# Kernel optimization log

Measured on AMD Instinct MI355X. Metric: run time of the kernel, lower is better.

Reference implementation:

```python
import jax, jax.numpy as jnp
import numpy as np
import itertools, math

# Static config (matches init_kwargs)
DIM = 384
KEY_DIM = 16
NUM_HEADS = 8
ATTN_RATIO = 4
RES = 14
OUT_DIM = 768
RES2 = math.ceil(RES / 2)          # 7
N = RES * RES                      # 196
N2 = RES2 * RES2                   # 49
D = ATTN_RATIO * KEY_DIM           # 64
NH_KD = NUM_HEADS * KEY_DIM        # 128
DH = NUM_HEADS * D                 # 512
SCALE = KEY_DIM ** -0.5
BATCH = 512


def _build_bias_idxs():
    points = list(itertools.product(range(RES), range(RES)))
    points_ = list(itertools.product(range(RES2), range(RES2)))
    ratio = math.ceil(RES / RES2)
    offsets = {}
    idxs = []
    for p1 in points_:
        for p2 in points:
            off = (abs(p1[0] * ratio - p2[0]), abs(p1[1] * ratio - p2[1]))
            if off not in offsets:
                offsets[off] = len(offsets)
            idxs.append(offsets[off])
    return np.array(idxs, dtype=np.int32).reshape(N2, N), len(offsets)


def setup_inputs() -> dict:
    key = jax.random.key(0)
    ks = jax.random.split(key, 16)
    idxs_np, n_off = _build_bias_idxs()
    w = lambda k, shape, s=0.05: (jax.random.normal(k, shape, jnp.float32) * s)
    inp = {
        "x": jax.random.normal(ks[0], (BATCH, DIM, RES, RES), jnp.float32),
        # LGQuery: depthwise 3x3 s2 conv (groups=DIM), then 1x1 conv + BN (folded scale/shift)
        "q_local_w": w(ks[1], (DIM, 1, 3, 3)),
        "q_local_b": w(ks[2], (DIM,)),
        "q_proj_w": w(ks[3], (NH_KD, DIM)),
        "q_proj_b": w(ks[4], (NH_KD,)),
        "q_bn_s": 1.0 + w(ks[5], (NH_KD,)),
        "q_bn_t": w(ks[5], (NH_KD,)),
        # k: 1x1 conv + BN
        "k_w": w(ks[6], (NH_KD, DIM)),
        "k_b": w(ks[7], (NH_KD,)),
        "k_bn_s": 1.0 + w(ks[8], (NH_KD,)),
        "k_bn_t": w(ks[8], (NH_KD,)),
        # v: 1x1 conv + BN
        "v_w": w(ks[9], (DH, DIM)),
        "v_b": w(ks[10], (DH,)),
        "v_bn_s": 1.0 + w(ks[10], (DH,)),
        "v_bn_t": w(ks[10], (DH,)),
        # v_local: depthwise 3x3 s2 (groups=DH) + BN
        "vl_w": w(ks[11], (DH, 1, 3, 3)),
        "vl_b": w(ks[12], (DH,)),
        "vl_bn_s": 1.0 + w(ks[12], (DH,)),
        "vl_bn_t": w(ks[12], (DH,)),
        # proj: GELU -> 1x1 conv -> BN
        "p_w": w(ks[13], (OUT_DIM, DH)),
        "p_b": w(ks[14], (OUT_DIM,)),
        "p_bn_s": 1.0 + w(ks[14], (OUT_DIM,)),
        "p_bn_t": w(ks[14], (OUT_DIM,)),
        # learned relative-position biases + gather indices
        "attn_biases": w(ks[15], (NUM_HEADS, n_off), 0.02),
        "bias_idxs": jnp.asarray(idxs_np),  # [N2, N] int32
    }
    return inp


def _dwconv_s2(x, w, b):
    # depthwise 3x3, stride 2, pad 1, NCHW
    C = x.shape[1]
    y = jax.lax.conv_general_dilated(
        x, w, window_strides=(2, 2), padding=((1, 1), (1, 1)),
        feature_group_count=C, dimension_numbers=("NCHW", "OIHW", "NCHW"))
    return y + b[None, :, None, None]


def _conv1x1_bn(x, w, b, s, t):
    y = jnp.einsum("bchw,oc->bohw", x, w) + b[None, :, None, None]
    return y * s[None, :, None, None] + t[None, :, None, None]


def reference(x, q_local_w, q_local_b, q_proj_w, q_proj_b, q_bn_s, q_bn_t,
              k_w, k_b, k_bn_s, k_bn_t, v_w, v_b, v_bn_s, v_bn_t,
              vl_w, vl_b, vl_bn_s, vl_bn_t, p_w, p_b, p_bn_s, p_bn_t,
              attn_biases, bias_idxs):
    B = x.shape[0]
    # LGQuery: depthwise conv + avgpool(k=1,s=2)==stride subsample, then 1x1+BN
    ql = _dwconv_s2(x, q_local_w, q_local_b) + x[:, :, ::2, ::2]
    q = _conv1x1_bn(ql, q_proj_w, q_proj_b, q_bn_s, q_bn_t)        # [B,128,7,7]
    q = q.reshape(B, NUM_HEADS, KEY_DIM, N2).transpose(0, 1, 3, 2)  # bhqc

    k = _conv1x1_bn(x, k_w, k_b, k_bn_s, k_bn_t).reshape(B, NUM_HEADS, KEY_DIM, N)  # bhck

    v4 = _conv1x1_bn(x, v_w, v_b, v_bn_s, v_bn_t)                   # [B,512,14,14]
    v_local = _dwconv_s2(v4, vl_w, vl_b)
    v_local = v_local * vl_bn_s[None, :, None, None] + vl_bn_t[None, :, None, None]
    v = v4.reshape(B, NUM_HEADS, D, N).transpose(0, 1, 3, 2)        # bhkd

    bias = attn_biases[:, bias_idxs]                                # [H,N2,N]
    attn = jax.nn.softmax(jnp.einsum("bhqc,bhck->bhqk", q, k) * SCALE + bias[None], axis=-1)
    out = jnp.einsum("bhqk,bhkd->bhqd", attn, v)                    # [B,H,N2,D]
    out = out.transpose(0, 1, 3, 2).reshape(B, DH, RES2, RES2) + v_local
    out = jax.nn.gelu(out, approximate=False)                       # torch nn.GELU default (erf)
    out = _conv1x1_bn(out, p_w, p_b, p_bn_s, p_bn_t)                # [B,768,7,7]
    return out
```

## Files before the change

### kernel.cpp

```cpp
#include <hip/hip_runtime.h>
#include <math.h>

#define DIM 384
#define NUM_HEADS 8
#define RES 14
#define RES2 7
#define NPOS 196
#define N2 49
#define DHEAD 64
#define NH_KD 128
#define DH 512
#define OUT_DIM 768
#define BATCH 512
#define SCALE_Q 0.25f

typedef unsigned short u16;
typedef short s16x8 __attribute__((ext_vector_type(8)));
typedef short s16x4 __attribute__((ext_vector_type(4)));
typedef float f32x4 __attribute__((ext_vector_type(4)));
typedef unsigned int u32x2 __attribute__((ext_vector_type(2)));

__device__ __forceinline__ float bf2f(u16 u) {
  union { unsigned int i; float f; } v; v.i = ((unsigned int)u) << 16; return v.f;
}
__device__ __forceinline__ u16 f2bf(float f) {
  union { unsigned int i; float f; } v; v.f = f;
  unsigned int r = v.i + 0x7fffu + ((v.i >> 16) & 1u);
  return (u16)(r >> 16);
}

#define GLD16(gp, lp) __builtin_amdgcn_global_load_lds( \
    (const __attribute__((address_space(1))) void*)(gp), \
    (__attribute__((address_space(3))) void*)(lp), 16, 0, 0)

__global__ __launch_bounds__(256) void k_prep(const float* __restrict__ kw, const float* __restrict__ vw,
                                              const float* __restrict__ qw, const float* __restrict__ pw,
                                              const float* __restrict__ ab, const int* __restrict__ idxs, int noff,
                                              u16* __restrict__ kwb, u16* __restrict__ vwb,
                                              u16* __restrict__ qwb, u16* __restrict__ pwb,
                                              float* __restrict__ bxp) {
  int i = blockIdx.x * 256 + threadIdx.x;
  const int e1 = NH_KD * DIM;
  const int e2 = e1 + DH * DIM;
  const int e3 = e2 + NH_KD * DIM;
  const int e4 = e3 + OUT_DIM * DH;
  const int e5 = e4 + NUM_HEADS * N2 * 256;
  if (i < e1) kwb[i] = f2bf(kw[i]);
  else if (i < e2) vwb[i - e1] = f2bf(vw[i - e1]);
  else if (i < e3) qwb[i - e2] = f2bf(qw[i - e2]);
  else if (i < e4) pwb[i - e3] = f2bf(pw[i - e3]);
  else if (i < e5) {
    int j = i - e4;
    int f = j & 15, c = (j >> 4) & 15;
    int m = (j >> 8) % N2, h = j / (N2 * 256);
    int n = f * 16 + c;
    bxp[j] = (n < NPOS) ? ab[h * noff + idxs[m * NPOS + n]] : 0.f;
  }
}

__global__ __launch_bounds__(256) void k_transpose_dwq(const float* __restrict__ x, u16* __restrict__ xt,
                                                       const float* __restrict__ qlw, const float* __restrict__ qlb,
                                                       u16* __restrict__ qlt) {
  int b = blockIdx.y, c0 = blockIdx.x * 64;
  __shared__ __align__(8) u16 tileT[196 * 70];
  __shared__ float wlds2[576];
  __shared__ float blds[64];
  int tid = threadIdx.x;
  const float* xb = x + (size_t)b * DIM * NPOS;

  for (int idx = tid; idx < 64 * 49; idx += 256) {
    int ch = idx / 49, p4 = idx - ch * 49;
    f32x4 v = *(const f32x4*)(xb + (size_t)(c0 + ch) * NPOS + p4 * 4);
#pragma unroll
    for (int j = 0; j < 4; j++)
      tileT[(p4 * 4 + j) * 70 + ch] = f2bf(v[j]);
  }
  for (int i = tid; i < 576; i += 256) {
    int c = i / 9, t = i % 9;
    wlds2[t * 64 + c] = qlw[(size_t)(c0 + c) * 9 + t];
  }
  if (tid < 64) blds[tid] = qlb[c0 + tid];
  __syncthreads();

  u16* xtb = xt + (size_t)b * NPOS * DIM + c0;
  for (int idx = tid; idx < NPOS * 8; idx += 256) {
    int n = idx >> 3, g = (idx & 7) << 3;
    s16x8 val;
    ((uint*)&val)[0] = *(const uint*)&tileT[n * 70 + g];
    ((uint*)&val)[1] = *(const uint*)&tileT[n * 70 + g + 2];
    ((uint*)&val)[2] = *(const uint*)&tileT[n * 70 + g + 4];
    ((uint*)&val)[3] = *(const uint*)&tileT[n * 70 + g + 6];
    *(s16x8*)(xtb + (size_t)n * DIM + g) = val;
  }
  u16* qb = qlt + (size_t)b * N2 * DIM + c0;
  for (int idx = tid; idx < N2 * 32; idx += 256) {
    int cp = idx & 31, n2 = idx >> 5;
    int c = cp << 1;
    int r = n2 / RES2, s = n2 % RES2;
    uint rv = *(const uint*)&tileT[((2 * r) * RES + 2 * s) * 70 + c];
    float a0 = blds[c]     + bf2f((u16)(rv & 0xffff));
    float a1 = blds[c + 1] + bf2f((u16)(rv >> 16));
#pragma unroll
    for (int dy = 0; dy < 3; dy++) {
      int ry = 2 * r - 1 + dy;
      if (ry < 0 || ry >= RES) continue;
#pragma unroll
      for (int dx = 0; dx < 3; dx++) {
        int sx = 2 * s - 1 + dx;
        if (sx < 0 || sx >= RES) continue;
        uint tv = *(const uint*)&tileT[(ry * RES + sx) * 70 + c];
        int t = dy * 3 + dx;
        a0 += wlds2[t * 64 + c]     * bf2f((u16)(tv & 0xffff));
        a1 += wlds2[t * 64 + c + 1] * bf2f((u16)(tv >> 16));
      }
    }
    uint outp = (uint)f2bf(a0) | ((uint)f2bf(a1) << 16);
    *(uint*)(qb + (size_t)n2 * DIM + c) = outp;
  }
}

template <int SPLN, bool F32OUT>
__global__ __launch_bounds__(256) void k_gemm_flat(
    const u16* __restrict__ A, const u16* __restrict__ B, void* __restrict__ C,
    const float* __restrict__ cb, const float* __restrict__ bns, const float* __restrict__ bnt,
    int K, int NMT, int ldc, long bstride) {
  __shared__ __align__(16) u16 a_lds[2 * 128 * 32];
  __shared__ __align__(16) u16 b_lds[2 * 128 * 32];
  int nwg = gridDim.x, bx = blockIdx.x;
  int wg = ((nwg & 7) == 0) ? ((bx & 7) * (nwg >> 3) + (bx >> 3)) : bx;
  int mt = wg % NMT, nt = wg / NMT;
  int m0 = mt * 128, n0 = nt * 128;
  int tid = threadIdx.x, w = tid >> 6, l = tid & 63;

  int srow = l >> 2;
  int scol = ((l & 3) ^ ((l >> 3) & 3)) * 8;
  const u16* asrc[2]; const u16* bsrc[2];
#pragma unroll
  for (int c = 0; c < 2; c++) {
    int chunk = w * 2 + c;
    asrc[c] = A + (size_t)(m0 + chunk * 16 + srow) * K + scol;
    bsrc[c] = B + (size_t)(n0 + chunk * 16 + srow) * K + scol;
  }
  char* adst = (char*)a_lds + (w * 2) * 1024 + l * 16;
  char* bdst = (char*)b_lds + (w * 2) * 1024 + l * 16;

  f32x4 acc[4][4];
#pragma unroll
  for (int i = 0; i < 4; i++)
#pragma unroll
    for (int j = 0; j < 4; j++) acc[i][j] = (f32x4){0.f, 0.f, 0.f, 0.f};

  int wm = w >> 1, wn = w & 1;
  int rg8 = ((l >> 4) ^ ((l >> 1) & 3)) * 8;
  int arow = wm * 64 + (l & 15);
  int brow = wn * 64 + (l & 15);

  for (int kk = 0; kk < K; kk += 64) {
#pragma unroll
    for (int c = 0; c < 2; c++) {
      GLD16(asrc[c] + kk,      adst + c * 1024);
      GLD16(asrc[c] + kk + 32, adst + 8192 + c * 1024);
      GLD16(bsrc[c] + kk,      bdst + c * 1024);
      GLD16(bsrc[c] + kk + 32, bdst + 8192 + c * 1024);
    }
    __syncthreads();
#pragma unroll
    for (int hf = 0; hf < 2; hf++) {
      const u16* ah = a_lds + hf * (128 * 32);
      const u16* bh = b_lds + hf * (128 * 32);
      s16x8 af[4], bf[4];
#pragma unroll
      for (int i = 0; i < 4; i++) {
        af[i] = *(const s16x8*)(&ah[(arow + i * 16) * 32 + rg8]);
        bf[i] = *(const s16x8*)(&bh[(brow + i * 16) * 32 + rg8]);
      }
#pragma unroll
      for (int i = 0; i < 4; i++)
#pragma unroll
        for (int j = 0; j < 4; j++)
          acc[i][j] = __builtin_amdgcn_mfma_f32_16x16x32_bf16(af[i], bf[j], acc[i][j], 0, 0, 0);
    }
    __syncthreads();
  }

  int ncol = l & 15, mq = (l >> 4) * 4;
#pragma unroll
  for (int i = 0; i < 4; i++) {
#pragma unroll
    for (int j = 0; j < 4; j++) {
      int n = n0 + wn * 64 + j * 16 + ncol;
#pragma unroll
      for (int r = 0; r < 4; r++) {
        int m = m0 + wm * 64 + i * 16 + mq + r;
        int ch = SPLN ? m : n;
        float val = acc[i][j][r] * bns[ch] + (cb[ch] * bns[ch] + bnt[ch]);
        size_t o;
        if (SPLN) o = (size_t)(n / SPLN) * bstride + (size_t)m * SPLN + (n % SPLN);
        else      o = (size_t)m * ldc + n;
        if (F32OUT) ((float*)C)[o] = val;
        else        ((u16*)C)[o] = f2bf(val);
      }
    }
  }
}

__global__ __launch_bounds__(256) void k_dwconv_v(const u16* __restrict__ v4, const float* __restrict__ w,
    const float* __restrict__ bias, const float* __restrict__ bns, const float* __restrict__ bnt,
    u16* __restrict__ vlt) {
  int b = blockIdx.y, ct = blockIdx.x;
  __shared__ u16 tile[64][196];
  int tid = threadIdx.x, wave = tid >> 6, lane = tid & 63;
  const u16* vbp = v4 + ((size_t)b * DH + ct * 64) * NPOS;
  for (int r = wave; r < 64; r += 4) {
    const u16* row = vbp + (size_t)r * NPOS;
    tile[r][lane]       = row[lane];
    tile[r][lane + 64]  = row[lane + 64];
    tile[r][lane + 128] = row[lane + 128];
    if (lane < 4) tile[r][lane + 192] = row[lane + 192];
  }
  __syncthreads();
  for (int idx = tid; idx < 64 * N2; idx += 256) {
    int cl = idx & 63, n2 = idx >> 6;
    int ch = ct * 64 + cl;
    int r = n2 / RES2, s = n2 % RES2;
    float acc = bias[ch];
#pragma unroll
    for (int dy = 0; dy < 3; dy++) {
      int ry = 2 * r - 1 + dy;
      if (ry < 0 || ry >= RES) continue;
#pragma unroll
      for (int dx = 0; dx < 3; dx++) {
        int sx = 2 * s - 1 + dx;
        if (sx < 0 || sx >= RES) continue;
        acc += w[ch * 9 + dy * 3 + dx] * bf2f(tile[cl][ry * RES + sx]);
      }
    }
    vlt[((size_t)b * N2 + n2) * DH + ch] = f2bf(acc * bns[ch] + bnt[ch]);
  }
}

__global__ __launch_bounds__(256, 4) void k_attn_mfma(const u16* __restrict__ qT, const u16* __restrict__ kT,
    const u16* __restrict__ v4, const float* __restrict__ bxp, const u16* __restrict__ vlT,
    u16* __restrict__ gT) {
  int h = blockIdx.x, b = blockIdx.y;
  __shared__ __align__(16) u16 p_lds[64 * 232];
  float* o_lds = (float*)p_lds;
  int tid = threadIdx.x, w = tid >> 6, l = tid & 63;
  int part = l >> 4, row16 = l & 15;
  int mbase = w * 16 + part * 4;
  int ncol = l & 15;

  for (int idx = tid; idx < 64 * 8; idx += 256)
    ((uint*)&p_lds[(idx >> 3) * 232])[104 + (idx & 7)] = 0;

  s16x8 af = (s16x8){0, 0, 0, 0, 0, 0, 0, 0};
  if (part < 2)
    af = *(const s16x8*)(qT + ((size_t)b * N2 + (w * 16 + row16)) * NH_KD + h * 16 + part * 8);

  const u16* kbase = kT + (size_t)b * NPOS * NH_KD + h * 16 + part * 8;
  f32x4 s[13];
#pragma unroll
  for (int f = 0; f < 13; f++) {
    s16x8 bf = (s16x8){0, 0, 0, 0, 0, 0, 0, 0};
    if (part < 2)
      bf = *(const s16x8*)(kbase + (size_t)(f * 16 + row16) * NH_KD);
    s[f] = __builtin_amdgcn_mfma_f32_16x16x32_bf16(af, bf, (f32x4){0.f, 0.f, 0.f, 0.f}, 0, 0, 0);
  }

  const u16* vbase = v4 + ((size_t)b * DH + h * DHEAD) * NPOS;
  int vd = l & 15, vq8 = part * 8;
  auto VLOAD = [&](int f, int kk) {
    const u16* p = vbase + (size_t)(f * 16 + vd) * NPOS + kk + vq8;
    s16x8 r;
    ((u32x2*)&r)[0] = *(const u32x2*)(p);
    ((u32x2*)&r)[1] = *(const u32x2*)(p + 4);
    return r;
  };
  s16x8 vb0[4];
#pragma unroll
  for (int f = 0; f < 4; f++) vb0[f] = VLOAD(f, 0);

#pragma unroll
  for (int q = 0; q < 4; q++) {
    f32x4 bqr[4];
#pragma unroll
    for (int r = 0; r < 4; r++) {
      int mm = mbase + r; if (mm > N2 - 1) mm = N2 - 1;
      bqr[r] = *(const f32x4*)(bxp + (((size_t)h * N2 + mm) * 16 + ncol) * 16 + q * 4);
    }
#pragma unroll
    for (int ff = 0; ff < 4; ff++) {
      int f = q * 4 + ff;
      if (f < 13) {
        int n = f * 16 + ncol;
#pragma unroll
        for (int r = 0; r < 4; r++) {
          int m = mbase + r;
          s[f][r] = (m < N2 && n < NPOS) ? s[f][r] * SCALE_Q + bqr[r][ff] : -1e30f;
        }
      }
    }
  }
#pragma unroll
  for (int r = 0; r < 4; r++) {
    float mx = s[0][r];
#pragma unroll
    for (int f = 1; f < 13; f++) mx = fmaxf(mx, s[f][r]);
    mx = fmaxf(mx, __shfl_xor(mx, 1)); mx = fmaxf(mx, __shfl_xor(mx, 2));
    mx = fmaxf(mx, __shfl_xor(mx, 4)); mx = fmaxf(mx, __shfl_xor(mx, 8));
    float sum = 0.f;
#pragma unroll
    for (int f = 0; f < 13; f++) { s[f][r] = __expf(s[f][r] - mx); sum += s[f][r]; }
    sum += __shfl_xor(sum, 1); sum += __shfl_xor(sum, 2);
    sum += __shfl_xor(sum, 4); sum += __shfl_xor(sum, 8);
    float inv = 1.f / sum;
#pragma unroll
    for (int f = 0; f < 13; f++) s[f][r] *= inv;
  }
#pragma unroll
  for (int f = 0; f < 13; f++) {
    int n = f * 16 + ncol;
#pragma unroll
    for (int r = 0; r < 4; r++)
      p_lds[(mbase + r) * 232 + n] = f2bf(s[f][r]);
  }
  __syncthreads();

  f32x4 o[4];
#pragma unroll
  for (int f = 0; f < 4; f++) o[f] = (f32x4){0.f, 0.f, 0.f, 0.f};
#pragma unroll
  for (int t = 0; t < 7; t++) {
    int kk = t * 32;
    s16x8 vn[4];
    if (t < 6) {
#pragma unroll
      for (int f = 0; f < 4; f++) vn[f] = VLOAD(f, kk + 32);
    }
    s16x8 pa = *(const s16x8*)(&p_lds[(w * 16 + row16) * 232 + kk + part * 8]);
#pragma unroll
    for (int f = 0; f < 4; f++)
      o[f] = __builtin_amdgcn_mfma_f32_16x16x32_bf16(pa, vb0[f], o[f], 0, 0, 0);
    if (t < 6) {
#pragma unroll
      for (int f = 0; f < 4; f++) vb0[f] = vn[f];
    }
  }
  __syncthreads();

#pragma unroll
  for (int f = 0; f < 4; f++)
#pragma unroll
    for (int r = 0; r < 4; r++) {
      int m = mbase + r;
      if (m < N2) o_lds[m * 68 + f * 16 + ncol] = o[f][r];
    }
  __syncthreads();

  for (int idx = tid; idx < N2 * 16; idx += 256) {
    int row = idx >> 4, c4 = (idx & 15) << 2;
    f32x4 ov = *(const f32x4*)(&o_lds[row * 68 + c4]);
    size_t go = ((size_t)b * N2 + row) * DH + h * DHEAD + c4;
    s16x4 vv = *(const s16x4*)(vlT + go);
    s16x4 outv;
#pragma unroll
    for (int e = 0; e < 4; e++) {
      float xv = ov[e] + bf2f((u16)vv[e]);
      float g = 0.5f * xv * (1.f + erff(xv * 0.70710678118f));
      outv[e] = (short)f2bf(g);
    }
    *(s16x4*)(gT + go) = outv;
  }
}

extern "C" void kernel_launch(void* const* d_in, const int* in_sizes, int n_in,
                              void* d_out, int out_size, void* d_ws, size_t ws_size,
                              hipStream_t stream) {
  const float* x   = (const float*)d_in[0];
  const float* qlw = (const float*)d_in[1];
  const float* qlb = (const float*)d_in[2];
  const float* qpw = (const float*)d_in[3];
  const float* qpb = (const float*)d_in[4];
  const float* qbs = (const float*)d_in[5];
  const float* qbt = (const float*)d_in[6];
  const float* kw  = (const float*)d_in[7];
  const float* kb  = (const float*)d_in[8];
  const float* kbs = (const float*)d_in[9];
  const float* kbt = (const float*)d_in[10];
  const float* vw  = (const float*)d_in[11];
  const float* vb  = (const float*)d_in[12];
  const float* vbs = (const float*)d_in[13];
  const float* vbt = (const float*)d_in[14];
  const float* vlw = (const float*)d_in[15];
  const float* vlb = (const float*)d_in[16];
  const float* vls = (const float*)d_in[17];
  const float* vlt_in = (const float*)d_in[18];
  const float* pw  = (const float*)d_in[19];
  const float* pb  = (const float*)d_in[20];
  const float* pbs = (const float*)d_in[21];
  const float* pbt = (const float*)d_in[22];
  const float* ab  = (const float*)d_in[23];
  const int*   bidx = (const int*)d_in[24];
  int noff = in_sizes[23] / NUM_HEADS;

  char* ws = (char*)d_ws;
  size_t off = 0;
  auto alloc = [&](size_t bytes) { char* p = ws + off; off += (bytes + 255) & ~(size_t)255; return p; };
  u16* xbT = (u16*)alloc((size_t)BATCH * NPOS * DIM * 2);
  u16* kTm = (u16*)alloc((size_t)BATCH * NPOS * NH_KD * 2);
  u16* qlT = (u16*)alloc((size_t)BATCH * N2 * DIM * 2);
  u16* qTm = (u16*)alloc((size_t)BATCH * N2 * NH_KD * 2);
  u16* v4m = (u16*)alloc((size_t)BATCH * DH * NPOS * 2);
  u16* vlTm = (u16*)alloc((size_t)BATCH * N2 * DH * 2);
  float* bxp = (float*)alloc((size_t)NUM_HEADS * N2 * 16 * 16 * 4);
  u16* kwb = (u16*)alloc((size_t)NH_KD * DIM * 2);
  u16* vwb = (u16*)alloc((size_t)DH * DIM * 2);
  u16* qwb = (u16*)alloc((size_t)NH_KD * DIM * 2);
  u16* pwb = (u16*)alloc((size_t)OUT_DIM * DH * 2);
  u16* gTm = xbT;

  k_prep<<<(788480 + 255) / 256, 256, 0, stream>>>(kw, vw, qpw, pw, ab, bidx, noff,
                                                   kwb, vwb, qwb, pwb, bxp);

  k_transpose_dwq<<<dim3(6, BATCH), 256, 0, stream>>>(x, xbT, qlw, qlb, qlT);

  k_gemm_flat<0, false><<<784, 256, 0, stream>>>(
      xbT, kwb, kTm, kb, kbs, kbt, DIM, 784, NH_KD, 0);
  k_gemm_flat<NPOS, false><<<3136, 256, 0, stream>>>(
      vwb, xbT, v4m, vb, vbs, vbt, DIM, 4, 0, (long)DH * NPOS);
  k_gemm_flat<0, false><<<196, 256, 0, stream>>>(
      qlT, qwb, qTm, qpb, qbs, qbt, DIM, 196, NH_KD, 0);

  k_dwconv_v<<<dim3(8, BATCH), 256, 0, stream>>>(v4m, vlw, vlb, vls, vlt_in, vlTm);
  k_attn_mfma<<<dim3(NUM_HEADS, BATCH), 256, 0, stream>>>(qTm, kTm, v4m, bxp, vlTm, gTm);

  k_gemm_flat<N2, true><<<1176, 256, 0, stream>>>(
      pwb, gTm, d_out, pb, pbs, pbt, DH, 6, 0, (long)OUT_DIM * N2);
}
```

Baseline: 379.5 us.

## Load small weight operand directly from global, vectorize dwconv tile load, fast GELU

Adds an ADIRECT mode to the flat GEMM in which the A operand (the small weight matrix) is read straight from global/L2 into registers, bypassing LDS staging. This cuts LDS traffic and the A-side load instructions for the V projection and the output projection. The depthwise conv tile load now uses 8-byte vector loads instead of scalar u16 loads. The exact erf GELU is replaced with an Abramowitz-Stegun polynomial approximation using a hardware reciprocal and fast exp, which trades a small accuracy loss for fewer instructions.

```diff
diff --git a/kernel.cpp b/kernel.cpp
--- a/kernel.cpp
+++ b/kernel.cpp
@@ -27,6 +27,17 @@
   union { unsigned int i; float f; } v; v.f = f;
   unsigned int r = v.i + 0x7fffu + ((v.i >> 16) & 1u);
   return (u16)(r >> 16);
+}
+
+__device__ __forceinline__ float gelu_f(float x) {
+  float z = x * 0.70710678118f;
+  float az = fabsf(z);
+  float t = __builtin_amdgcn_rcpf(1.f + 0.3275911f * az);
+  float p = ((((1.061405429f * t - 1.453152027f) * t + 1.421413741f) * t
+              - 0.284496736f) * t + 0.254829592f) * t;
+  float erfv = 1.f - p * __expf(-az * az);
+  erfv = copysignf(erfv, z);
+  return 0.5f * x * (1.f + erfv);
 }
 
 #define GLD16(gp, lp) __builtin_amdgcn_global_load_lds( \
@@ -119,12 +130,12 @@
   }
 }
 
-template <int SPLN, bool F32OUT>
+template <int SPLN, bool F32OUT, bool ADIRECT>
 __global__ __launch_bounds__(256) void k_gemm_flat(
     const u16* __restrict__ A, const u16* __restrict__ B, void* __restrict__ C,
     const float* __restrict__ cb, const float* __restrict__ bns, const float* __restrict__ bnt,
     int K, int NMT, int ldc, long bstride) {
-  __shared__ __align__(16) u16 a_lds[2 * 128 * 32];
+  __shared__ __align__(16) u16 a_lds[ADIRECT ? 8 : 2 * 128 * 32];
   __shared__ __align__(16) u16 b_lds[2 * 128 * 32];
   int nwg = gridDim.x, bx = blockIdx.x;
   int wg = ((nwg & 7) == 0) ? ((bx & 7) * (nwg >> 3) + (bx >> 3)) : bx;
@@ -138,10 +149,10 @@
 #pragma unroll
   for (int c = 0; c < 2; c++) {
     int chunk = w * 2 + c;
-    asrc[c] = A + (size_t)(m0 + chunk * 16 + srow) * K + scol;
+    if (!ADIRECT) asrc[c] = A + (size_t)(m0 + chunk * 16 + srow) * K + scol;
     bsrc[c] = B + (size_t)(n0 + chunk * 16 + srow) * K + scol;
   }
-  char* adst = (char*)a_lds + (w * 2) * 1024 + l * 16;
+  char* adst = ADIRECT ? nullptr : (char*)a_lds + (w * 2) * 1024 + l * 16;
   char* bdst = (char*)b_lds + (w * 2) * 1024 + l * 16;
 
   f32x4 acc[4][4];
@@ -154,12 +165,15 @@
   int rg8 = ((l >> 4) ^ ((l >> 1) & 3)) * 8;
   int arow = wm * 64 + (l & 15);
   int brow = wn * 64 + (l & 15);
+  const u16* afp = A + (size_t)(m0 + wm * 64 + (l & 15)) * K + (l >> 4) * 8;
 
   for (int kk = 0; kk < K; kk += 64) {
 #pragma unroll
     for (int c = 0; c < 2; c++) {
-      GLD16(asrc[c] + kk,      adst + c * 1024);
-      GLD16(asrc[c] + kk + 32, adst + 8192 + c * 1024);
+      if (!ADIRECT) {
+        GLD16(asrc[c] + kk,      adst + c * 1024);
+        GLD16(asrc[c] + kk + 32, adst + 8192 + c * 1024);
+      }
       GLD16(bsrc[c] + kk,      bdst + c * 1024);
       GLD16(bsrc[c] + kk + 32, bdst + 8192 + c * 1024);
     }
@@ -171,7 +185,8 @@
       s16x8 af[4], bf[4];
 #pragma unroll
       for (int i = 0; i < 4; i++) {
-        af[i] = *(const s16x8*)(&ah[(arow + i * 16) * 32 + rg8]);
+        if (ADIRECT) af[i] = *(const s16x8*)(afp + (size_t)i * 16 * K + kk + hf * 32);
+        else         af[i] = *(const s16x8*)(&ah[(arow + i * 16) * 32 + rg8]);
         bf[i] = *(const s16x8*)(&bh[(brow + i * 16) * 32 + rg8]);
       }
 #pragma unroll
@@ -208,15 +223,12 @@
     const float* __restrict__ bias, const float* __restrict__ bns, const float* __restrict__ bnt,
     u16* __restrict__ vlt) {
   int b = blockIdx.y, ct = blockIdx.x;
-  __shared__ u16 tile[64][196];
+  __shared__ __align__(8) u16 tile[64][196];
   int tid = threadIdx.x, wave = tid >> 6, lane = tid & 63;
   const u16* vbp = v4 + ((size_t)b * DH + ct * 64) * NPOS;
   for (int r = wave; r < 64; r += 4) {
-    const u16* row = vbp + (size_t)r * NPOS;
-    tile[r][lane]       = row[lane];
-    tile[r][lane + 64]  = row[lane + 64];
-    tile[r][lane + 128] = row[lane + 128];
-    if (lane < 4) tile[r][lane + 192] = row[lane + 192];
+    const u32x2* grow = (const u32x2*)(vbp + (size_t)r * NPOS);
+    if (lane < 49) ((u32x2*)&tile[r][0])[lane] = grow[lane];
   }
   __syncthreads();
   for (int idx = tid; idx < 64 * N2; idx += 256) {
@@ -366,8 +378,7 @@
 #pragma unroll
     for (int e = 0; e < 4; e++) {
       float xv = ov[e] + bf2f((u16)vv[e]);
-      float g = 0.5f * xv * (1.f + erff(xv * 0.70710678118f));
-      outv[e] = (short)f2bf(g);
+      outv[e] = (short)f2bf(gelu_f(xv));
     }
     *(s16x4*)(gT + go) = outv;
   }
@@ -424,16 +435,16 @@
 
   k_transpose_dwq<<<dim3(6, BATCH), 256, 0, stream>>>(x, xbT, qlw, qlb, qlT);
 
-  k_gemm_flat<0, false><<<784, 256, 0, stream>>>(
+  k_gemm_flat<0, false, false><<<784, 256, 0, stream>>>(
       xbT, kwb, kTm, kb, kbs, kbt, DIM, 784, NH_KD, 0);
-  k_gemm_flat<NPOS, false><<<3136, 256, 0, stream>>>(
+  k_gemm_flat<NPOS, false, true><<<3136, 256, 0, stream>>>(
       vwb, xbT, v4m, vb, vbs, vbt, DIM, 4, 0, (long)DH * NPOS);
-  k_gemm_flat<0, false><<<196, 256, 0, stream>>>(
+  k_gemm_flat<0, false, false><<<196, 256, 0, stream>>>(
       qlT, qwb, qTm, qpb, qbs, qbt, DIM, 196, NH_KD, 0);
 
   k_dwconv_v<<<dim3(8, BATCH), 256, 0, stream>>>(v4m, vlw, vlb, vls, vlt_in, vlTm);
   k_attn_mfma<<<dim3(NUM_HEADS, BATCH), 256, 0, stream>>>(qTm, kTm, v4m, bxp, vlTm, gTm);
 
-  k_gemm_flat<N2, true><<<1176, 256, 0, stream>>>(
+  k_gemm_flat<N2, true, true><<<1176, 256, 0, stream>>>(
       pwb, gTm, d_out, pb, pbs, pbt, DH, 6, 0, (long)OUT_DIM * N2);
 }
```

New measurement: 430.4 us. 1.13x slower.
